# Kernel tuning notes

Measured on AMD Instinct MI355X. Metric: run time of the kernel, lower is better.

Reference implementation:

```python
import jax, jax.numpy as jnp
import numpy as np

ASSIGN_TEMP = 0.1
BATCH_SIZE = 16
NUM_PROTOTYPES = 1024
EMBD_DIM = 512


def setup_inputs() -> dict:
    key = jax.random.key(0)
    k1, k2 = jax.random.split(key)
    feature_maps = jax.random.normal(k1, (BATCH_SIZE, EMBD_DIM, 64, 64), dtype=jnp.float32)
    prototypes = jax.random.normal(k2, (1, NUM_PROTOTYPES, EMBD_DIM), dtype=jnp.float32)
    return {"feature_maps": feature_maps, "prototypes": prototypes}


def reference(feature_maps, prototypes):
    # assign_nearest_clusters
    bs, c, h, w = feature_maps.shape
    K = prototypes.shape[1]
    # [N, c] pixel embeddings (channels-last flatten, as movedim(1,3).reshape)
    x = feature_maps.transpose(0, 2, 3, 1).reshape(-1, c)
    p = prototypes[0]  # [K, c]
    d2 = (jnp.sum(x * x, axis=1, keepdims=True)
          + jnp.sum(p * p, axis=1)[None, :]
          - 2.0 * (x @ p.T))
    dist = jnp.sqrt(jnp.maximum(d2, 0.0))  # [N, K]
    sims = jax.nn.softmax(-dist / ASSIGN_TEMP, axis=1)  # [N, K]
    sims = sims.reshape(bs, h, w, K).transpose(0, 3, 1, 2)  # [bs, K, h, w]
    nearest = jnp.argmax(sims, axis=1)  # [bs, h, w]
    onehot = jax.nn.one_hot(nearest, K, dtype=jnp.int32)  # [bs, h, w, K]
    counts = onehot.sum(axis=(1, 2))  # [bs, K] pixels per prototype
    mask = (counts > 3).sum()
    return sims, mask.astype(jnp.float32) / BATCH_SIZE
```

## Files before the change

kernel.cpp:

```cpp
#include <hip/hip_runtime.h>
#include <hip/hip_bf16.h>
#include <stdint.h>

typedef _Float16 f16x8 __attribute__((ext_vector_type(8)));
typedef _Float16 f16x4 __attribute__((ext_vector_type(4)));
typedef _Float16 f16x2 __attribute__((ext_vector_type(2)));
typedef float    f32x4 __attribute__((ext_vector_type(4)));

#define NPROTO 1024
#define EMB    512
#define NB     16
#define HW     4096
#define NPIX   (NB * HW)
#define INV_TEMP 10.0f
#define NSLICE 8

__global__ void prep_protos(const float* __restrict__ proto,
                            _Float16* __restrict__ Ph,
                            float* __restrict__ pnorm) {
    int k = blockIdx.x;
    int t = threadIdx.x;
    const float* src = proto + (size_t)k * EMB + t * 8;
    float4 v0 = ((const float4*)src)[0];
    float4 v1 = ((const float4*)src)[1];
    float sq = v0.x*v0.x + v0.y*v0.y + v0.z*v0.z + v0.w*v0.w
             + v1.x*v1.x + v1.y*v1.y + v1.z*v1.z + v1.w*v1.w;
    f16x8 h;
    h[0] = (_Float16)v0.x; h[1] = (_Float16)v0.y; h[2] = (_Float16)v0.z; h[3] = (_Float16)v0.w;
    h[4] = (_Float16)v1.x; h[5] = (_Float16)v1.y; h[6] = (_Float16)v1.z; h[7] = (_Float16)v1.w;
    *(f16x8*)(Ph + (size_t)k * EMB + t * 8) = h;
#pragma unroll
    for (int m = 1; m < 64; m <<= 1) sq += __shfl_xor(sq, m);
    if (t == 0) pnorm[k] = sq;
}

__global__ void zero_counts(int* __restrict__ counts) {
    int i = blockIdx.x * blockDim.x + threadIdx.x;
    if (i < NB * NPROTO) counts[i] = 0;
}

__global__ __launch_bounds__(1024)
void p0_transpose(const float* __restrict__ fm, _Float16* __restrict__ Xh,
                  float* __restrict__ xn) {
    __shared__ __align__(16) unsigned char tile[128 * 1024];
    __shared__ float xnpart[32 * 128];

    const int t   = threadIdx.x;
    const int b   = blockIdx.x >> 5;
    const int px0 = (blockIdx.x & 31) * 128;

    float sq0 = 0.f, sq1 = 0.f, sq2 = 0.f, sq3 = 0.f;
    const int p4 = t & 31;
#pragma unroll
    for (int j = 0; j < 16; ++j) {
        int f4 = j * 1024 + t;
        int c  = f4 >> 5;
        float4 v = *(const float4*)(fm + ((size_t)b * EMB + c) * HW + px0 + p4 * 4);
        sq0 += v.x * v.x; sq1 += v.y * v.y; sq2 += v.z * v.z; sq3 += v.w * v.w;
#pragma unroll
        for (int i = 0; i < 4; ++i) {
            int p = p4 * 4 + i;
            float val = (i == 0) ? v.x : (i == 1) ? v.y : (i == 2) ? v.z : v.w;
            int slot = (c >> 3) ^ ((p >> 2) & 63);
            *(_Float16*)(tile + p * 1024 + slot * 16 + (c & 7) * 2) = (_Float16)val;
        }
    }
    xnpart[(t >> 5) * 128 + p4 * 4 + 0] = sq0;
    xnpart[(t >> 5) * 128 + p4 * 4 + 1] = sq1;
    xnpart[(t >> 5) * 128 + p4 * 4 + 2] = sq2;
    xnpart[(t >> 5) * 128 + p4 * 4 + 3] = sq3;
    __syncthreads();

    if (t < 128) {
        float s = 0.f;
#pragma unroll
        for (int g = 0; g < 32; ++g) s += xnpart[g * 128 + t];
        xn[b * HW + px0 + t] = s;
    }
    const int wid = t >> 6, lane = t & 63;
#pragma unroll
    for (int rr = 0; rr < 8; ++rr) {
        int p = wid * 8 + rr;
        int phys = lane ^ ((p >> 2) & 63);
        f16x8 v = *(const f16x8*)(tile + p * 1024 + phys * 16);
        *(f16x8*)(Xh + ((size_t)b * HW + px0 + p) * EMB + lane * 8) = v;
    }
}

__global__ __launch_bounds__(256, 4)
void pA_gemm(const _Float16* __restrict__ Xh, const _Float16* __restrict__ Ph,
             const float* __restrict__ pnorm, const float* __restrict__ xn,
             _Float16* __restrict__ e_out, float4* __restrict__ pstat) {
    __shared__ __align__(16) unsigned char smem[33280];
    float* pn = (float*)(smem + 32768);
    float* redsum = (float*)(smem);
    float* argv_  = (float*)(smem + 1024);
    int*   argk_  = (int*)(smem + 2048);

    const int t    = threadIdx.x;
    const int lane = t & 63, wid = t >> 6;
    const int kw   = wid >> 1, pw = wid & 1;
    const int lrow = lane >> 4, lcol = lane & 15;

    const int pt    = blockIdx.x >> 3, slice = blockIdx.x & 7;
    const int gpx0  = pt * 128;
    const int k0g   = slice * 128;

    if (t < 128) pn[t] = pnorm[k0g + t];

    f32x4 acc[4][4];
#pragma unroll
    for (int i = 0; i < 4; ++i)
#pragma unroll
        for (int j = 0; j < 4; ++j)
#pragma unroll
            for (int e = 0; e < 4; ++e) acc[i][j][e] = 0.0f;

    const int srow = t >> 2, sslot = t & 3;
    auto stage = [&](int buf, int ks) {
        const int c0 = ks * 32;
#pragma unroll
        for (int p = 0; p < 2; ++p) {
            int row = p * 64 + srow;
            int cg  = sslot ^ ((row >> 1) & 3);
            __builtin_amdgcn_global_load_lds(
                (const __attribute__((address_space(1))) void*)(Ph + (size_t)(k0g + row) * EMB + c0 + cg * 8),
                (__attribute__((address_space(3))) void*)(smem + buf * 16384 + p * 4096 + wid * 1024),
                16, 0, 0);
            __builtin_amdgcn_global_load_lds(
                (const __attribute__((address_space(1))) void*)(Xh + (size_t)(gpx0 + row) * EMB + c0 + cg * 8),
                (__attribute__((address_space(3))) void*)(smem + buf * 16384 + 8192 + p * 4096 + wid * 1024),
                16, 0, 0);
        }
    };

    stage(0, 0);
    __syncthreads();

#pragma unroll
    for (int ks = 0; ks < 16; ++ks) {
        const unsigned char* cb = smem + (ks & 1) * 16384;
        if (ks < 15) stage((ks & 1) ^ 1, ks + 1);

        f16x8 bf[4];
#pragma unroll
        for (int nf = 0; nf < 4; ++nf) {
            int px = pw * 64 + nf * 16 + lcol;
            bf[nf] = *(const f16x8*)(cb + 8192 + px * 64 + ((lrow ^ ((px >> 1) & 3)) << 4));
        }
        __builtin_amdgcn_s_setprio(1);
#pragma unroll
        for (int mf = 0; mf < 4; ++mf) {
            int r = kw * 64 + mf * 16 + lcol;
            f16x8 af = *(const f16x8*)(cb + r * 64 + ((lrow ^ ((r >> 1) & 3)) << 4));
#pragma unroll
            for (int nf = 0; nf < 4; ++nf)
                acc[mf][nf] = __builtin_amdgcn_mfma_f32_16x16x32_f16(af, bf[nf], acc[mf][nf], 0, 0, 0);
        }
        __builtin_amdgcn_s_setprio(0);
        __syncthreads();
    }

    float xnv[4];
#pragma unroll
    for (int nf = 0; nf < 4; ++nf) xnv[nf] = xn[gpx0 + pw * 64 + nf * 16 + lcol];

    float lav[4] = {-1e30f, -1e30f, -1e30f, -1e30f};
    int   lak[4] = {0, 0, 0, 0};
#pragma unroll
    for (int mf = 0; mf < 4; ++mf) {
        const int klb = kw * 64 + mf * 16 + lrow * 4;
        float4 pn4 = *(const float4*)(pn + klb);
#pragma unroll
        for (int nf = 0; nf < 4; ++nf)
#pragma unroll
            for (int j = 0; j < 4; ++j) {
                float pnj = (j == 0) ? pn4.x : (j == 1) ? pn4.y : (j == 2) ? pn4.z : pn4.w;
                float d2 = fmaxf(xnv[nf] + pnj - 2.0f * acc[mf][nf][j], 0.0f);
                float sq;
                asm("v_sqrt_f32 %0, %1" : "=v"(sq) : "v"(d2));
                float lg = -INV_TEMP * sq;
                acc[mf][nf][j] = lg;
                if (lg > lav[nf]) { lav[nf] = lg; lak[nf] = klb + j; }
            }
    }
#pragma unroll
    for (int nf = 0; nf < 4; ++nf)
#pragma unroll
        for (int m = 16; m <= 32; m <<= 1) {
            float ov = __shfl_xor(lav[nf], m);
            int   ok = __shfl_xor(lak[nf], m);
            if (ov > lav[nf] || (ov == lav[nf] && ok < lak[nf])) { lav[nf] = ov; lak[nf] = ok; }
        }
    if (lane < 16)
#pragma unroll
        for (int nf = 0; nf < 4; ++nf) {
            int px = pw * 64 + nf * 16 + lane;
            argv_[kw * 128 + px] = lav[nf];
            argk_[kw * 128 + px] = lak[nf];
        }
    __syncthreads();

#pragma unroll
    for (int nf = 0; nf < 4; ++nf) {
        int px = pw * 64 + nf * 16 + lcol;
        float m = fmaxf(argv_[px], argv_[128 + px]);
        float s = 0.0f;
#pragma unroll
        for (int mf = 0; mf < 4; ++mf)
#pragma unroll
            for (int j = 0; j < 4; ++j) {
                float e = __expf(acc[mf][nf][j] - m);
                acc[mf][nf][j] = e;
                s += e;
            }
        s += __shfl_xor(s, 16);
        s += __shfl_xor(s, 32);
        if (lane < 16) redsum[kw * 128 + nf * 16 + pw * 64 + lane] = s;
    }

#pragma unroll
    for (int mf = 0; mf < 4; ++mf)
#pragma unroll
        for (int nf = 0; nf < 4; ++nf) {
            int px = pw * 64 + nf * 16 + lcol;
            int kl = kw * 64 + mf * 16 + lrow * 4;
            f16x4 h;
#pragma unroll
            for (int j = 0; j < 4; ++j) h[j] = (_Float16)acc[mf][nf][j];
            *(f16x4*)(e_out + (size_t)(gpx0 + px) * NPROTO + k0g + kl) = h;
        }
    __syncthreads();

    if (kw == 0 && lane < 16) {
#pragma unroll
        for (int nf = 0; nf < 4; ++nf) {
            int px = pw * 64 + nf * 16 + lane;
            float av = argv_[px]; int ak = argk_[px];
            float a1 = argv_[128 + px]; int k1 = argk_[128 + px];
            if (a1 > av) { av = a1; ak = k1; }
            float s = redsum[px] + redsum[128 + px];
            float4 st;
            st.x = av; st.y = s; st.z = __int_as_float(k0g + ak); st.w = 0.0f;
            pstat[(size_t)slice * NPIX + gpx0 + px] = st;
        }
    }
}

__global__ void pC_combine(const float4* __restrict__ pstat, float* __restrict__ scale,
                           int* __restrict__ counts) {
    int px = blockIdx.x * 256 + threadIdx.x;
    if (px >= NPIX) return;
    float4 st[NSLICE];
#pragma unroll
    for (int s = 0; s < NSLICE; ++s) st[s] = pstat[(size_t)s * NPIX + px];
    float m = -1e30f;
#pragma unroll
    for (int s = 0; s < NSLICE; ++s) m = fmaxf(m, st[s].x);
    float es[NSLICE];
    float S = 0.0f;
#pragma unroll
    for (int s = 0; s < NSLICE; ++s) { es[s] = __expf(st[s].x - m); S += st[s].y * es[s]; }
    float rs = 1.0f / S;
#pragma unroll
    for (int s = 0; s < NSLICE; ++s) scale[(size_t)px * NSLICE + s] = es[s] * rs;
    float bv = st[0].x; int bk = __float_as_int(st[0].z);
#pragma unroll
    for (int s = 1; s < NSLICE; ++s)
        if (st[s].x > bv) { bv = st[s].x; bk = __float_as_int(st[s].z); }
    int b = px >> 12;
    atomicAdd(&counts[b * NPROTO + bk], 1);
}

__global__ __launch_bounds__(1024)
void pB_emit(const _Float16* __restrict__ e, const float* __restrict__ scale,
             float* __restrict__ out) {
    __shared__ float tile[64 * 261];

    const int t = threadIdx.x;
    const int px0g = blockIdx.x * 256;
    const int b = px0g >> 12, hw0 = px0g & 4095;
    const int lpx = t >> 2, kq = t & 3;
    const int orow = t >> 4, oseg = t & 15;

    for (int kc = 0; kc < 16; ++kc) {
        int slice = kc >> 1;
        float sc = scale[(size_t)(px0g + lpx) * NSLICE + slice];
        const _Float16* src = e + (size_t)(px0g + lpx) * NPROTO + kc * 64 + kq * 16;
        f16x8 h0 = *(const f16x8*)(src);
        f16x8 h1 = *(const f16x8*)(src + 8);
        if (kc) __syncthreads();
#pragma unroll
        for (int j = 0; j < 8; ++j) {
            tile[(kq * 16 + j) * 261 + lpx]     = (float)h0[j] * sc;
            tile[(kq * 16 + 8 + j) * 261 + lpx] = (float)h1[j] * sc;
        }
        __syncthreads();
        size_t obase = (size_t)b * NPROTO * HW + (size_t)(kc * 64 + orow) * HW + hw0 + oseg * 16;
#pragma unroll
        for (int i = 0; i < 4; ++i) {
            float4 v;
            v.x = tile[orow * 261 + oseg * 16 + i * 4 + 0];
            v.y = tile[orow * 261 + oseg * 16 + i * 4 + 1];
            v.z = tile[orow * 261 + oseg * 16 + i * 4 + 2];
            v.w = tile[orow * 261 + oseg * 16 + i * 4 + 3];
            *(float4*)(out + obase + i * 4) = v;
        }
    }
}

__global__ void finalize(const int* __restrict__ counts, float* __restrict__ out) {
    int t = threadIdx.x;
    int local = 0;
    for (int i = t; i < NB * NPROTO; i += 256) local += (counts[i] > 3) ? 1 : 0;
#pragma unroll
    for (int m = 1; m < 64; m <<= 1) local += __shfl_xor(local, m);
    __shared__ int wsum[4];
    if ((t & 63) == 0) wsum[t >> 6] = local;
    __syncthreads();
    if (t == 0) out[(size_t)NPIX * NPROTO] = (float)(wsum[0] + wsum[1] + wsum[2] + wsum[3]) / 16.0f;
}

__global__ __launch_bounds__(1024, 1)
void assign_fused(const float* __restrict__ fm, const _Float16* __restrict__ Ph,
                  const float* __restrict__ pnorm, int* __restrict__ counts,
                  float* __restrict__ out) {
    __shared__ __align__(16) unsigned char smem[143360];
    unsigned char* Abuf = smem;
    unsigned char* Bbuf = smem + 131072;
    float* pn           = (float*)(smem + 139264);
    float* redmax = (float*)(smem);
    float* redsum = (float*)(smem + 4096);
    float* argv_  = (float*)(smem + 8192);
    int*   argk_  = (int*)  (smem + 12288);
    float* xnsum  = (float*)(smem + 16384);
    float* xn     = (float*)(smem + 20480);

    const int t    = threadIdx.x;
    const int lane = t & 63, wid = t >> 6;
    const int lrow = lane >> 4, lcol = lane & 15;
    const int n0  = blockIdx.x * 64;
    const int b   = n0 >> 12;
    const int hw0 = n0 & 4095;

    pn[t] = pnorm[t];
    f32x4 acc[4][4];
#pragma unroll
    for (int i = 0; i < 4; ++i)
#pragma unroll
        for (int j = 0; j < 4; ++j)
#pragma unroll
            for (int e = 0; e < 4; ++e) acc[i][j][e] = 0.0f;

    const int bpx = t & 63;
    const int bc  = (t >> 6) << 1;
    const float* fmB = fm + (size_t)b * EMB * HW + hw0 + bpx;
    float sq = 0.0f;
    float bv0, bv1;

    auto stageA = [&](int cur, int ks) {
        const int c0 = ks * 32;
#pragma unroll
        for (int p = 0; p < 4; ++p) {
            int k  = p * 256 + wid * 16 + (lane >> 2);
            int cg = (lane & 3) ^ (k & 3);
            __builtin_amdgcn_global_load_lds(
                (const __attribute__((address_space(1))) void*)(Ph + (size_t)k * EMB + c0 + cg * 8),
                (__attribute__((address_space(3))) void*)(Abuf + cur * 65536 + p * 16384 + wid * 1024),
                16, 0, 0);
        }
    };
    auto loadB = [&](int ks) {
        const float* p0 = fmB + (size_t)(ks * 32 + bc) * HW;
        bv0 = p0[0]; bv1 = p0[HW];
    };
    auto writeB = [&](int cur) {
        sq += bv0 * bv0 + bv1 * bv1;
        f16x2 h; h[0] = (_Float16)bv0; h[1] = (_Float16)bv1;
        int slot = (bc >> 3) ^ (bpx & 3);
        *(f16x2*)(Bbuf + cur * 4096 + bpx * 64 + (slot << 4) + (bc & 7) * 2) = h;
    };

    stageA(0, 0); loadB(0); writeB(0);
    __syncthreads();
    int cur = 0;
    for (int ks = 0; ks < 16; ++ks) {
        if (ks < 15) { stageA(cur ^ 1, ks + 1); loadB(ks + 1); }
        f16x8 bf[4];
#pragma unroll
        for (int nf = 0; nf < 4; ++nf) {
            int px = nf * 16 + lcol;
            bf[nf] = *(const f16x8*)(Bbuf + cur * 4096 + px * 64 + ((lrow ^ (px & 3)) << 4));
        }
#pragma unroll
        for (int mf = 0; mf < 4; ++mf) {
            int r = wid * 64 + mf * 16 + lcol;
            f16x8 af = *(const f16x8*)(Abuf + cur * 65536 + r * 64 + ((lrow ^ (r & 3)) << 4));
#pragma unroll
            for (int nf = 0; nf < 4; ++nf)
                acc[mf][nf] = __builtin_amdgcn_mfma_f32_16x16x32_f16(af, bf[nf], acc[mf][nf], 0, 0, 0);
        }
        if (ks < 15) writeB(cur ^ 1);
        __syncthreads();
        cur ^= 1;
    }

    xnsum[(t >> 6) * 64 + bpx] = sq;
    __syncthreads();
    if (t < 64) {
        float s = 0.0f;
#pragma unroll
        for (int g = 0; g < 16; ++g) s += xnsum[g * 64 + t];
        xn[t] = s;
    }
    __syncthreads();

    float xnv[4];
#pragma unroll
    for (int nf = 0; nf < 4; ++nf) xnv[nf] = xn[nf * 16 + lcol];
    float lmax[4] = {-1e30f, -1e30f, -1e30f, -1e30f};
    float lav[4]  = {-1e30f, -1e30f, -1e30f, -1e30f};
    int   lak[4]  = {0, 0, 0, 0};
#pragma unroll
    for (int mf = 0; mf < 4; ++mf)
#pragma unroll
        for (int nf = 0; nf < 4; ++nf)
#pragma unroll
            for (int j = 0; j < 4; ++j) {
                int kidx = wid * 64 + mf * 16 + lrow * 4 + j;
                float d2 = xnv[nf] + pn[kidx] - 2.0f * acc[mf][nf][j];
                float lg = -INV_TEMP * sqrtf(fmaxf(d2, 0.0f));
                acc[mf][nf][j] = lg;
                if (lg > lav[nf]) { lav[nf] = lg; lak[nf] = kidx; }
                lmax[nf] = fmaxf(lmax[nf], lg);
            }
#pragma unroll
    for (int nf = 0; nf < 4; ++nf)
#pragma unroll
        for (int m = 16; m <= 32; m <<= 1) {
            float ov = __shfl_xor(lav[nf], m);
            int   ok = __shfl_xor(lak[nf], m);
            if (ov > lav[nf] || (ov == lav[nf] && ok < lak[nf])) { lav[nf] = ov; lak[nf] = ok; }
            lmax[nf] = fmaxf(lmax[nf], __shfl_xor(lmax[nf], m));
        }
    if (lane < 16)
#pragma unroll
        for (int nf = 0; nf < 4; ++nf) {
            int idx = wid * 64 + nf * 16 + lane;
            redmax[idx] = lmax[nf]; argv_[idx] = lav[nf]; argk_[idx] = lak[nf];
        }
    __syncthreads();

#pragma unroll
    for (int nf = 0; nf < 4; ++nf) {
        int px = nf * 16 + lcol;
        float gm = -1e30f, gav = -1e30f;
        int gak = 0;
#pragma unroll
        for (int w = 0; w < 16; ++w) {
            gm = fmaxf(gm, redmax[w * 64 + px]);
            float av = argv_[w * 64 + px];
            int   ak = argk_[w * 64 + px];
            if (av > gav || (av == gav && ak < gak)) { gav = av; gak = ak; }
        }
        if (wid == 0 && lane < 16) atomicAdd(&counts[b * NPROTO + gak], 1);
        float s = 0.0f;
#pragma unroll
        for (int mf = 0; mf < 4; ++mf)
#pragma unroll
            for (int j = 0; j < 4; ++j) {
                float e = __expf(acc[mf][nf][j] - gm);
                acc[mf][nf][j] = e;
                s += e;
            }
        s += __shfl_xor(s, 16);
        s += __shfl_xor(s, 32);
        if (lane < 16) redsum[wid * 64 + nf * 16 + lane] = s;
    }
    __syncthreads();

    const size_t obase = (size_t)b * NPROTO * HW + hw0;
#pragma unroll
    for (int nf = 0; nf < 4; ++nf) {
        int px = nf * 16 + lcol;
        float s = 0.0f;
#pragma unroll
        for (int w = 0; w < 16; ++w) s += redsum[w * 64 + px];
        float inv = 1.0f / s;
#pragma unroll
        for (int mf = 0; mf < 4; ++mf)
#pragma unroll
            for (int j = 0; j < 4; ++j) {
                int kidx = wid * 64 + mf * 16 + lrow * 4 + j;
                out[obase + (size_t)kidx * HW + px] = acc[mf][nf][j] * inv;
            }
    }
}

extern "C" void kernel_launch(void* const* d_in, const int* in_sizes, int n_in,
                              void* d_out, int out_size, void* d_ws, size_t ws_size,
                              hipStream_t stream) {
    const float* fm    = (const float*)d_in[0];
    const float* proto = (const float*)d_in[1];
    float* out = (float*)d_out;

    char* ws = (char*)d_ws;
    const size_t E_OFF  = 0;
    const size_t XH_OFF = 134217728;
    const size_t PS_OFF = XH_OFF + 67108864;
    const size_t SC_OFF = PS_OFF + 8388608;
    const size_t XN_OFF = SC_OFF + 2097152;
    const size_t PH_OFF = XN_OFF + 262144;
    const size_t PN_OFF = PH_OFF + 1048576;
    const size_t CT_OFF = PN_OFF + 4096;
    const size_t NEED   = CT_OFF + 65536;

    if (ws_size >= NEED) {
        _Float16* e     = (_Float16*)(ws + E_OFF);
        _Float16* Xh    = (_Float16*)(ws + XH_OFF);
        float4*   pstat = (float4*)(ws + PS_OFF);
        float*    scale = (float*)(ws + SC_OFF);
        float*    xn    = (float*)(ws + XN_OFF);
        _Float16* Ph    = (_Float16*)(ws + PH_OFF);
        float*    pnorm = (float*)(ws + PN_OFF);
        int*      counts= (int*)(ws + CT_OFF);

        prep_protos<<<NPROTO, 64, 0, stream>>>(proto, Ph, pnorm);
        zero_counts<<<(NB * NPROTO + 255) / 256, 256, 0, stream>>>(counts);
        p0_transpose<<<NB * 32, 1024, 0, stream>>>(fm, Xh, xn);
        pA_gemm<<<(NPIX / 128) * NSLICE, 256, 0, stream>>>(Xh, Ph, pnorm, xn, e, pstat);
        pC_combine<<<NPIX / 256, 256, 0, stream>>>(pstat, scale, counts);
        pB_emit<<<NPIX / 256, 1024, 0, stream>>>(e, scale, out);
        finalize<<<1, 256, 0, stream>>>(counts, out);
    } else {
        _Float16* Ph    = (_Float16*)ws;
        float*    pnorm = (float*)(ws + (size_t)NPROTO * EMB * 2);
        int*      counts= (int*)(ws + (size_t)NPROTO * EMB * 2 + 4096);
        prep_protos<<<NPROTO, 64, 0, stream>>>(proto, Ph, pnorm);
        zero_counts<<<(NB * NPROTO + 255) / 256, 256, 0, stream>>>(counts);
        assign_fused<<<NPIX / 64, 1024, 0, stream>>>(fm, Ph, pnorm, counts, out);
        finalize<<<1, 256, 0, stream>>>(counts, out);
    }
}
```

Baseline: 329.6 us.

## Stage softmax exp tile through LDS for coalesced 16-byte output stores

The exp values are now written into a swizzled LDS tile and then read back so each thread writes 16-byte f16x8 chunks along the prototype dimension, replacing the scattered 8-byte f16x4 global stores. The reduction scratch buffers move past the tile region, which raises the LDS footprint. Global load pointers for the double-buffered staging are precomputed and incremented instead of recomputing addresses each step. The aim is better write coalescing for the large e_out tensor, at the cost of an extra LDS round trip and more shared memory, which may affect occupancy.

Result: faster. 300.6 us (-8.8%).

```diff
diff --git a/kernel.cpp b/kernel.cpp
--- a/kernel.cpp
+++ b/kernel.cpp
@@ -91,11 +91,11 @@
 void pA_gemm(const _Float16* __restrict__ Xh, const _Float16* __restrict__ Ph,
              const float* __restrict__ pnorm, const float* __restrict__ xn,
              _Float16* __restrict__ e_out, float4* __restrict__ pstat) {
-    __shared__ __align__(16) unsigned char smem[33280];
-    float* pn = (float*)(smem + 32768);
-    float* redsum = (float*)(smem);
-    float* argv_  = (float*)(smem + 1024);
-    int*   argk_  = (int*)(smem + 2048);
+    __shared__ __align__(16) unsigned char smem[36352];
+    float* pn     = (float*)(smem + 32768);
+    float* redsum = (float*)(smem + 33280);
+    float* argv_  = (float*)(smem + 34304);
+    int*   argk_  = (int*)(smem + 35328);
 
     const int t    = threadIdx.x;
     const int lane = t & 63, wid = t >> 6;
@@ -117,30 +117,39 @@
             for (int e = 0; e < 4; ++e) acc[i][j][e] = 0.0f;
 
     const int srow = t >> 2, sslot = t & 3;
-    auto stage = [&](int buf, int ks) {
-        const int c0 = ks * 32;
-#pragma unroll
-        for (int p = 0; p < 2; ++p) {
-            int row = p * 64 + srow;
-            int cg  = sslot ^ ((row >> 1) & 3);
-            __builtin_amdgcn_global_load_lds(
-                (const __attribute__((address_space(1))) void*)(Ph + (size_t)(k0g + row) * EMB + c0 + cg * 8),
-                (__attribute__((address_space(3))) void*)(smem + buf * 16384 + p * 4096 + wid * 1024),
-                16, 0, 0);
-            __builtin_amdgcn_global_load_lds(
-                (const __attribute__((address_space(1))) void*)(Xh + (size_t)(gpx0 + row) * EMB + c0 + cg * 8),
-                (__attribute__((address_space(3))) void*)(smem + buf * 16384 + 8192 + p * 4096 + wid * 1024),
-                16, 0, 0);
-        }
+    const int scg  = sslot ^ ((srow >> 1) & 3);
+    const _Float16* pA0 = Ph + (size_t)(k0g + srow) * EMB + scg * 8;
+    const _Float16* pA1 = Ph + (size_t)(k0g + 64 + srow) * EMB + scg * 8;
+    const _Float16* pB0 = Xh + (size_t)(gpx0 + srow) * EMB + scg * 8;
+    const _Float16* pB1 = Xh + (size_t)(gpx0 + 64 + srow) * EMB + scg * 8;
+
+    auto stage = [&](int buf) {
+        unsigned char* base = smem + buf * 16384;
+        __builtin_amdgcn_global_load_lds(
+            (const __attribute__((address_space(1))) void*)pA0,
+            (__attribute__((address_space(3))) void*)(base + wid * 1024), 16, 0, 0);
+        __builtin_amdgcn_global_load_lds(
+            (const __attribute__((address_space(1))) void*)pB0,
+            (__attribute__((address_space(3))) void*)(base + 8192 + wid * 1024), 16, 0, 0);
+        __builtin_amdgcn_global_load_lds(
+            (const __attribute__((address_space(1))) void*)pA1,
+            (__attribute__((address_space(3))) void*)(base + 4096 + wid * 1024), 16, 0, 0);
+        __builtin_amdgcn_global_load_lds(
+            (const __attribute__((address_space(1))) void*)pB1,
+            (__attribute__((address_space(3))) void*)(base + 12288 + wid * 1024), 16, 0, 0);
     };
 
-    stage(0, 0);
+    stage(0);
+    pA0 += 32; pA1 += 32; pB0 += 32; pB1 += 32;
     __syncthreads();
 
 #pragma unroll
     for (int ks = 0; ks < 16; ++ks) {
         const unsigned char* cb = smem + (ks & 1) * 16384;
-        if (ks < 15) stage((ks & 1) ^ 1, ks + 1);
+        if (ks < 15) {
+            stage((ks & 1) ^ 1);
+            pA0 += 32; pA1 += 32; pB0 += 32; pB1 += 32;
+        }
 
         f16x8 bf[4];
 #pragma unroll
@@ -207,30 +216,44 @@
         float m = fmaxf(argv_[px], argv_[128 + px]);
         float s = 0.0f;
 #pragma unroll
-        for (int mf = 0; mf < 4; ++mf)
+        for (int mf = 0; mf < 4; ++mf) {
+            int kl = kw * 64 + mf * 16 + lrow * 4;
+            f16x4 h;
 #pragma unroll
             for (int j = 0; j < 4; ++j) {
                 float e = __expf(acc[mf][nf][j] - m);
-                acc[mf][nf][j] = e;
                 s += e;
+                h[j] = (_Float16)e;
             }
+            int slot = (kl >> 2) ^ (px & 31);
+            *(f16x4*)(smem + px * 256 + slot * 8) = h;
+        }
         s += __shfl_xor(s, 16);
         s += __shfl_xor(s, 32);
         if (lane < 16) redsum[kw * 128 + nf * 16 + pw * 64 + lane] = s;
     }
-
-#pragma unroll
-    for (int mf = 0; mf < 4; ++mf)
-#pragma unroll
-        for (int nf = 0; nf < 4; ++nf) {
-            int px = pw * 64 + nf * 16 + lcol;
-            int kl = kw * 64 + mf * 16 + lrow * 4;
-            f16x4 h;
-#pragma unroll
-            for (int j = 0; j < 4; ++j) h[j] = (_Float16)acc[mf][nf][j];
-            *(f16x4*)(e_out + (size_t)(gpx0 + px) * NPROTO + k0g + kl) = h;
-        }
-    __syncthreads();
+    __syncthreads();
+
+    {
+        const int pxr = lane >> 3;
+        const int k8  = (lane & 7) * 8;
+#pragma unroll
+        for (int it = 0; it < 4; ++it) {
+            int px = wid * 32 + it * 8 + pxr;
+#pragma unroll
+            for (int kh = 0; kh < 2; ++kh) {
+                int k0 = kh * 64 + k8;
+                int s0 = ((k0 >> 2)     ) ^ (px & 31);
+                int s1 = ((k0 >> 2) + 1 ) ^ (px & 31);
+                f16x4 lo = *(const f16x4*)(smem + px * 256 + s0 * 8);
+                f16x4 hi = *(const f16x4*)(smem + px * 256 + s1 * 8);
+                f16x8 v;
+                v[0] = lo[0]; v[1] = lo[1]; v[2] = lo[2]; v[3] = lo[3];
+                v[4] = hi[0]; v[5] = hi[1]; v[6] = hi[2]; v[7] = hi[3];
+                *(f16x8*)(e_out + (size_t)(gpx0 + px) * NPROTO + k0g + k0) = v;
+            }
+        }
+    }
 
     if (kw == 0 && lane < 16) {
 #pragma unroll
```
